# Kernel tuning notes

Measured on AMD Instinct MI355X. Metric: run time of the kernel, lower is better.

## Reference

```python
import jax, jax.numpy as jnp
import numpy as np

EPS_LN = 1e-12
EPS_BN = 1e-5


def layernorm(x, w, b):
    u = jnp.mean(x, axis=-1, keepdims=True)
    s = jnp.mean((x - u) ** 2, axis=-1, keepdims=True)
    return w * ((x - u) / jnp.sqrt(s + EPS_LN)) + b


def reps_block(x, ln1_w, ln1_b, lin_w, lin_b, ln2_w, ln2_b):
    # GRAPHLayerNorm -> (dropout, identity in eval) -> Linear -> ReLU -> GRAPHLayerNorm
    h = layernorm(x, ln1_w, ln1_b)
    h = jax.nn.relu(jnp.einsum('bnd,od->bno', h, lin_w) + lin_b)
    return layernorm(h, ln2_w, ln2_b)


def attend(x):
    # full dense self-attention: softmax(x x^T) x ; dropout is identity in eval
    scores = jnp.einsum('bnd,bmd->bnm', x, x)  # [B,4096,4096]
    attn = jax.nn.softmax(scores, axis=-1)
    return jnp.einsum('bnm,bmd->bnd', attn, x)


def setup_inputs() -> dict:
    key = jax.random.key(0)
    ks = jax.random.split(key, 8)
    B, C, H, W = 4, 512, 64, 64
    D = 512
    inp = {
        'T1': jax.random.normal(ks[0], (B, C, H, W), jnp.float32),
        'T2': jax.random.normal(ks[1], (B, C, H, W), jnp.float32),
        'w_conv3': jax.random.normal(ks[2], (1024, 1024, 3, 3), jnp.float32) * 0.01,
        'w_conv1': jax.random.normal(ks[3], (512, 1024, 1, 1), jnp.float32) * 0.03,
        'bn_gamma': jnp.ones((512,), jnp.float32),
        'bn_beta': jnp.zeros((512,), jnp.float32),
        'bn_mean': jnp.zeros((512,), jnp.float32),
        'bn_var': jnp.ones((512,), jnp.float32),
        'ln1_w': jnp.ones((D,), jnp.float32),
        'ln1_b': jnp.zeros((D,), jnp.float32),
        'lin_w': jax.random.normal(ks[4], (D, D), jnp.float32) * 0.04,
        'lin_b': jnp.zeros((D,), jnp.float32),
        'ln2_w': jnp.ones((D,), jnp.float32),
        'ln2_b': jnp.zeros((D,), jnp.float32),
    }
    return inp


def reference(T1, T2, w_conv3, w_conv1, bn_gamma, bn_beta, bn_mean, bn_var,
              ln1_w, ln1_b, lin_w, lin_b, ln2_w, ln2_b):
    B = T1.shape[0]
    X = jnp.concatenate((T1, T2), axis=1)  # [B,1024,64,64]
    dn = ('NCHW', 'OIHW', 'NCHW')
    X = jax.lax.conv_general_dilated(X, w_conv3, (1, 1), ((1, 1), (1, 1)), dimension_numbers=dn)
    X = jax.lax.conv_general_dilated(X, w_conv1, (1, 1), ((0, 0), (0, 0)), dimension_numbers=dn)  # [B,512,64,64]
    # BatchNorm (eval, running stats) + ReLU
    inv = (bn_gamma / jnp.sqrt(bn_var + EPS_BN))[None, :, None, None]
    X = jax.nn.relu(X * inv + (bn_beta - bn_mean * bn_gamma / jnp.sqrt(bn_var + EPS_BN))[None, :, None, None])
    x = X.transpose(0, 2, 3, 1).reshape(B, 4096, 512)
    # block 1
    rel = attend(x)
    rel = reps_block(x + rel, ln1_w, ln1_b, lin_w, lin_b, ln2_w, ln2_b)
    # block 2 (original code reuses self.reps_graph, i.e. SAME params)
    rel1 = attend(rel)
    rel1 = reps_block(rel + rel1, ln1_w, ln1_b, lin_w, lin_b, ln2_w, ln2_b)
    return rel1.reshape(B, 64, 64, 512).transpose(0, 3, 1, 2)  # [B,512,64,64]
```

## Files before the change

kernel.cpp:

```cpp
#include <hip/hip_runtime.h>
#include <stdint.h>

typedef float f32x4 __attribute__((ext_vector_type(4)));
typedef __bf16 bf16x8 __attribute__((ext_vector_type(8)));
typedef unsigned short u16;
typedef unsigned short u16x8 __attribute__((ext_vector_type(8)));

__device__ __forceinline__ float bf2f(u16 u){ unsigned int i = ((unsigned int)u)<<16; float f; __builtin_memcpy(&f,&i,4); return f; }
__device__ __forceinline__ u16 f2bf(float f){ unsigned int i; __builtin_memcpy(&i,&f,4); i += 0x7FFFu + ((i>>16)&1u); return (u16)(i>>16); }
__device__ __forceinline__ u16 f2h(float f){ _Float16 h = (_Float16)f; u16 b; __builtin_memcpy(&b,&h,2); return b; }
__device__ __forceinline__ float h2f(u16 b){ _Float16 h; __builtin_memcpy(&h,&b,2); return (float)h; }

__device__ __forceinline__ void gld16(const void* g, void* l){
  __builtin_amdgcn_global_load_lds(
      (const __attribute__((address_space(1))) void*)(uintptr_t)g,
      (__attribute__((address_space(3))) void*)(unsigned int)(uintptr_t)l, 16, 0, 0);
}

__global__ __launch_bounds__(256) void border_zero(u16* __restrict__ Xpad){
  const int n = blockIdx.y, p = blockIdx.x;
  int y, x;
  if (p < 66)        { y = 0;        x = p; }
  else if (p < 132)  { y = 65;       x = p - 66; }
  else if (p < 196)  { y = p - 131;  x = 0; }
  else               { y = p - 195;  x = 65; }
  ushort4 z = {0,0,0,0};
  *(ushort4*)(Xpad + (((long)n*66 + y)*66 + x)*1024 + threadIdx.x*4) = z;
}

__global__ __launch_bounds__(256) void pad_interior(const float* __restrict__ T1,
                                                    const float* __restrict__ T2,
                                                    u16* __restrict__ Xpad){
  const int n = blockIdx.z, ct = blockIdx.y, pt = blockIdx.x;
  const int t = threadIdx.x;
  const int c0 = ct*64, p0 = pt*64;
  const float* src = (c0 < 512) ? (T1 + ((long)n*512 + c0)*4096)
                                : (T2 + ((long)n*512 + (c0-512))*4096);
  __shared__ u16 lds[64][66];
  #pragma unroll
  for (int i=0;i<4;i++){
    int c = i*16 + (t>>4);
    int ch = t&15;
    float4 v = *(const float4*)(src + (long)c*4096 + p0 + ch*4);
    int p = ch*4;
    lds[p+0][c] = f2bf(v.x); lds[p+1][c] = f2bf(v.y);
    lds[p+2][c] = f2bf(v.z); lds[p+3][c] = f2bf(v.w);
  }
  __syncthreads();
  #pragma unroll
  for (int i=0;i<8;i++){
    int p = i*8 + (t>>5);
    int c2 = t&31;
    int pix = p0 + p; int yy = (pix>>6)+1, xx = (pix&63)+1;
    ushort2 val; val.x = lds[p][2*c2]; val.y = lds[p][2*c2+1];
    *(ushort2*)(Xpad + (((long)n*66 + yy)*66 + xx)*1024 + c0 + 2*c2) = val;
  }
}

__global__ __launch_bounds__(256) void prep_w3(const float* __restrict__ w3, u16* __restrict__ wk3t){
  const int o = blockIdx.x; const int t = threadIdx.x;
  __shared__ u16 lds[9216];
  const float* src = w3 + (long)o*9216;
  #pragma unroll
  for (int i=0;i<9;i++){
    int j = i*256 + t;
    float4 v = *(const float4*)(src + j*4);
    lds[j*4+0]=f2bf(v.x); lds[j*4+1]=f2bf(v.y); lds[j*4+2]=f2bf(v.z); lds[j*4+3]=f2bf(v.w);
  }
  __syncthreads();
  u16* dst = wk3t + (long)o*9216;
  #pragma unroll
  for (int i=0;i<36;i++){
    int j = i*256 + t; int tp = j>>10, ci = j&1023;
    dst[j] = lds[ci*9+tp];
  }
}

__global__ void prep_small(const float* __restrict__ w1, const float* __restrict__ bg,
                           const float* __restrict__ bb, const float* __restrict__ bm,
                           const float* __restrict__ bv, const float* __restrict__ linw,
                           u16* __restrict__ w1t, u16* __restrict__ lint,
                           float* __restrict__ bias1){
  const int b = blockIdx.x, t = threadIdx.x;
  if (b < 2048){
    long i = (long)b*256 + t;
    int o = (int)(i>>10);
    float inv = bg[o] / sqrtf(bv[o] + 1e-5f);
    w1t[i] = f2bf(w1[i]*inv);
  } else if (b < 3072){
    long i = (long)(b-2048)*256 + t;
    lint[i] = f2bf(linw[i]);
  } else {
    int o = (b-3072)*256 + t;
    float inv = bg[o]/sqrtf(bv[o]+1e-5f);
    bias1[o] = bb[o] - bm[o]*inv;
  }
}

__global__ __launch_bounds__(256) void row_norm(const u16* __restrict__ x, float* __restrict__ nrm){
  const int row = blockIdx.x*4 + (threadIdx.x>>6);
  const int lane = threadIdx.x & 63;
  u16x8 q = *(const u16x8*)(x + (long)row*512 + lane*8);
  float s = 0.f;
  #pragma unroll
  for (int j=0;j<8;j++){ float f = bf2f(q[j]); s += f*f; }
  #pragma unroll
  for (int off=32; off; off>>=1) s += __shfl_xor(s, off);
  if (lane==0) nrm[row] = s;
}

__global__ __launch_bounds__(256) void transpose_bf(const u16* __restrict__ src, u16* __restrict__ dst,
                                                    int R, int C, long sStr, long dStr){
  const int z = blockIdx.z;
  src += (long)z*sStr; dst += (long)z*dStr;
  const int r0 = blockIdx.x*64, c0 = blockIdx.y*64;
  const int t = threadIdx.x;
  __shared__ u16 lds[64][66];
  #pragma unroll
  for (int i=0;i<4;i++){
    int r = i*16 + (t>>4), ch = t&15;
    ushort4 v = *(const ushort4*)(src + (long)(r0+r)*C + c0 + ch*4);
    lds[r][ch*4+0]=v.x; lds[r][ch*4+1]=v.y; lds[r][ch*4+2]=v.z; lds[r][ch*4+3]=v.w;
  }
  __syncthreads();
  #pragma unroll
  for (int i=0;i<4;i++){
    int c = i*16 + (t>>4), ch = t&15;
    ushort4 v;
    v.x = lds[ch*4+0][c]; v.y = lds[ch*4+1][c]; v.z = lds[ch*4+2][c]; v.w = lds[ch*4+3][c];
    *(ushort4*)(dst + (long)(c0+c)*R + r0 + ch*4) = v;
  }
}

__global__ __launch_bounds__(256) void transpose_bf_f32(const u16* __restrict__ src, float* __restrict__ dst){
  const int z = blockIdx.z;
  src += (long)z*4096*512; dst += (long)z*512*4096;
  const int r0 = blockIdx.x*64, c0 = blockIdx.y*64;
  const int t = threadIdx.x;
  __shared__ u16 lds[64][66];
  #pragma unroll
  for (int i=0;i<4;i++){
    int r = i*16 + (t>>4), ch = t&15;
    ushort4 v = *(const ushort4*)(src + (long)(r0+r)*512 + c0 + ch*4);
    lds[r][ch*4+0]=v.x; lds[r][ch*4+1]=v.y; lds[r][ch*4+2]=v.z; lds[r][ch*4+3]=v.w;
  }
  __syncthreads();
  #pragma unroll
  for (int i=0;i<4;i++){
    int c = i*16 + (t>>4), ch = t&15;
    float4 v;
    v.x = bf2f(lds[ch*4+0][c]); v.y = bf2f(lds[ch*4+1][c]);
    v.z = bf2f(lds[ch*4+2][c]); v.w = bf2f(lds[ch*4+3][c]);
    *(float4*)(dst + (long)(c0+c)*4096 + r0 + ch*4) = v;
  }
}

template<int EPI, int CONV>
__global__ __launch_bounds__(512, 2) void gemm256(
    const u16* __restrict__ Ain, const u16* __restrict__ Btin, void* __restrict__ Cv,
    int K, int lda, int ldb, int ldc, const float* __restrict__ srowIn,
    u16* __restrict__ C0, u16* __restrict__ C1, u16* __restrict__ C2, u16* __restrict__ C3)
{
  extern __shared__ u16 sm[];
  const int t = threadIdx.x;
  const int lane = t & 63;
  const int wid = t >> 6;
  const int wr = wid >> 2, wc = wid & 3;

  long m0, n0;
  int byv = 0, bxv = 0;
  const u16* A; const u16* Bt; const float* srow; u16* Cz;
  if (EPI == 3){
    const int orig = blockIdx.x;
    const int swz = (orig & 7) * 68 + (orig >> 3);
    const int z = swz / 136;
    int p = swz % 136;
    int by = 0;
    while (p >= 16 - by){ p -= 16 - by; by++; }
    const int bx = by + p;
    byv = by; bxv = bx;
    m0 = (long)by * 256; n0 = (long)bx * 256;
    A = Ain + (long)z*4096*lda;
    Bt = A;
    srow = srowIn + (long)z*4096;
    Cz = (z==0)?C0:(z==1)?C1:(z==2)?C2:C3;
  } else {
    const int orig = blockIdx.y * gridDim.x + blockIdx.x;
    const int cpx = (gridDim.x * gridDim.y) >> 3;
    const int swz = (orig & 7) * cpx + (orig >> 3);
    const int bx = swz % gridDim.x;
    const int by = swz / gridDim.x;
    m0 = (long)by * 256; n0 = (long)bx * 256;
    A = Ain; Bt = Btin; srow = srowIn; Cz = (u16*)Cv;
  }

  const int row0 = t >> 2;
  const int cs0  = (t & 3) ^ ((row0 >> 1) & 3);

  const u16 *aB0, *aB1;
  if (CONV) {
    long m_ = m0 + row0;
    long pb0 = ((long)((int)(m_>>12)*66 + (int)((m_>>6)&63)))*66 + (int)(m_&63);
    m_ = m0 + row0 + 128;
    long pb1 = ((long)((int)(m_>>12)*66 + (int)((m_>>6)&63)))*66 + (int)(m_&63);
    aB0 = A + pb0*1024 + cs0*8;
    aB1 = A + pb1*1024 + cs0*8;
  } else {
    aB0 = A + (m0 + row0)*(long)lda + cs0*8;
    aB1 = A + (m0 + row0 + 128)*(long)lda + cs0*8;
  }
  const u16* bB0 = Bt + (n0 + row0)*(long)ldb + cs0*8;
  const u16* bB1 = Bt + (n0 + row0 + 128)*(long)ldb + cs0*8;

  auto issueA = [&](int sub, long aoff){
    u16* d = sm + sub*8192 + t*8;
    gld16(aB0 + aoff, d);
    gld16(aB1 + aoff, d + 4096);
  };
  auto issueB = [&](int sub, long boff){
    u16* d = sm + 32768 + sub*8192 + t*8;
    gld16(bB0 + boff, d);
    gld16(bB1 + boff, d + 4096);
  };
  auto conv_aoff = [&](int tile)->long {
    int kb = tile << 6;
    int tap = kb >> 10;
    int cb  = kb & 1023;
    int ky = (tap >= 6) ? 2 : (tap >= 3 ? 1 : 0);
    int kx = tap - ky*3;
    return (long)(ky*66 + kx)*1024 + cb;
  };

  const int frow = lane & 15;
  const int elemoff = (((lane>>4) ^ ((frow>>1)&3)) << 3);
  const int rAoff = (wr*128 + frow)*32 + elemoff;
  const int rBoff = (wc*64  + frow)*32 + elemoff;

  f32x4 acc[8][4] = {};

  {
    long a0 = CONV ? conv_aoff(0) : 0L;
    issueA(0, a0);
    issueB(0, 0);
    issueA(1, a0 + 32);
    issueB(1, 32);
  }

  const int NT = K >> 6;
  for (int tile = 0; tile < NT; ++tile) {
    const int b = tile & 1;
    const int nb2 = b ^ 1;
    const bool lastT = (tile == NT-1);
    long aoffN = 0, boffN = 0;
    if (!lastT) {
      aoffN = CONV ? conv_aoff(tile+1) : (long)(tile+1)*64;
      boffN = (long)(tile+1)*64;
    }

    asm volatile("s_waitcnt vmcnt(4)" ::: "memory");
    __builtin_amdgcn_s_barrier();
    __builtin_amdgcn_sched_barrier(0);

    {
      const u16* pA = sm + (b*2+0)*8192 + rAoff;
      const u16* pB = sm + 32768 + (b*2+0)*8192 + rBoff;
      bf16x8 bf[4];
      #pragma unroll
      for (int i=0;i<4;i++) bf[i] = *(const bf16x8*)(pB + i*512);
      {
        bf16x8 a[4];
        #pragma unroll
        for (int i=0;i<4;i++) a[i] = *(const bf16x8*)(pA + i*512);
        if (!lastT) issueA(nb2*2+0, aoffN);
        __builtin_amdgcn_s_setprio(1);
        #pragma unroll
        for (int mi=0;mi<4;mi++)
          #pragma unroll
          for (int ni=0;ni<4;ni++)
            acc[mi][ni] = __builtin_amdgcn_mfma_f32_16x16x32_bf16(a[mi], bf[ni], acc[mi][ni],0,0,0);
        __builtin_amdgcn_s_setprio(0);
      }
      {
        bf16x8 a[4];
        #pragma unroll
        for (int i=0;i<4;i++) a[i] = *(const bf16x8*)(pA + (4+i)*512);
        if (!lastT) issueB(nb2*2+0, boffN);
        __builtin_amdgcn_s_setprio(1);
        #pragma unroll
        for (int mi=0;mi<4;mi++)
          #pragma unroll
          for (int ni=0;ni<4;ni++)
            acc[4+mi][ni] = __builtin_amdgcn_mfma_f32_16x16x32_bf16(a[mi], bf[ni], acc[4+mi][ni],0,0,0);
        __builtin_amdgcn_s_setprio(0);
      }
    }

    if (lastT) asm volatile("s_waitcnt vmcnt(0)" ::: "memory");
    else       asm volatile("s_waitcnt vmcnt(4)" ::: "memory");
    __builtin_amdgcn_s_barrier();
    __builtin_amdgcn_sched_barrier(0);

    {
      const u16* pA = sm + (b*2+1)*8192 + rAoff;
      const u16* pB = sm + 32768 + (b*2+1)*8192 + rBoff;
      bf16x8 bf[4];
      #pragma unroll
      for (int i=0;i<4;i++) bf[i] = *(const bf16x8*)(pB + i*512);
      {
        bf16x8 a[4];
        #pragma unroll
        for (int i=0;i<4;i++) a[i] = *(const bf16x8*)(pA + i*512);
        if (!lastT) issueA(nb2*2+1, aoffN + 32);
        __builtin_amdgcn_s_setprio(1);
        #pragma unroll
        for (int mi=0;mi<4;mi++)
          #pragma unroll
          for (int ni=0;ni<4;ni++)
            acc[mi][ni] = __builtin_amdgcn_mfma_f32_16x16x32_bf16(a[mi], bf[ni], acc[mi][ni],0,0,0);
        __builtin_amdgcn_s_setprio(0);
      }
      {
        bf16x8 a[4];
        #pragma unroll
        for (int i=0;i<4;i++) a[i] = *(const bf16x8*)(pA + (4+i)*512);
        if (!lastT) issueB(nb2*2+1, boffN + 32);
        __builtin_amdgcn_s_setprio(1);
        #pragma unroll
        for (int mi=0;mi<4;mi++)
          #pragma unroll
          for (int ni=0;ni<4;ni++)
            acc[4+mi][ni] = __builtin_amdgcn_mfma_f32_16x16x32_bf16(a[mi], bf[ni], acc[4+mi][ni],0,0,0);
        __builtin_amdgcn_s_setprio(0);
      }
    }
  }

  const int crow0 = wr*128 + ((lane>>4)<<2);
  const int ccol0 = wc*64 + frow;

  #pragma unroll
  for (int mi=0;mi<8;mi++){
    #pragma unroll
    for (int ni=0;ni<4;ni++){
      long col = n0 + ccol0 + ni*16;
      #pragma unroll
      for (int r=0;r<4;r++){
        long row = m0 + crow0 + mi*16 + r;
        float v = acc[mi][ni][r];
        if (EPI==3) Cz[row*(long)ldc + col] = f2h(v - srow[row]);
        else        Cz[row*(long)ldc + col] = f2bf(v);
      }
    }
  }

  if (EPI == 3 && bxv != byv){
    __syncthreads();
    u16* lt = sm;
    float sc[4];
    #pragma unroll
    for (int ni=0;ni<4;ni++) sc[ni] = srow[n0 + ccol0 + ni*16];
    #pragma unroll
    for (int mi=0;mi<8;mi++){
      const int g = (crow0 + mi*16) >> 2;
      #pragma unroll
      for (int ni=0;ni<4;ni++){
        const int col_l = ccol0 + ni*16;
        ushort4 pk;
        #pragma unroll
        for (int r=0;r<4;r++) pk[r] = f2h(acc[mi][ni][r] - sc[ni]);
        *(ushort4*)(lt + col_l*256 + ((g ^ (col_l & 63))<<2)) = pk;
      }
    }
    __syncthreads();
    const int half = lane >> 5, l32 = lane & 31;
    #pragma unroll
    for (int ps=0; ps<16; ps++){
      const int R = ps*16 + wid*2 + half;
      const int u0 = ((l32<<1)    ) ^ (R & 63);
      const int u1 = ((l32<<1) | 1) ^ (R & 63);
      ushort4 a = *(const ushort4*)(lt + R*256 + (u0<<2));
      ushort4 b = *(const ushort4*)(lt + R*256 + (u1<<2));
      u16* dst = Cz + (n0 + R)*(long)ldc + m0 + (l32<<3);
      *(ushort4*)dst = a;
      *(ushort4*)(dst+4) = b;
    }
  }
}

template<int EPI>
__global__ __launch_bounds__(256, 2) void gemm128_deep(
    const u16* __restrict__ A, const u16* __restrict__ Bt, u16* __restrict__ C,
    const float* __restrict__ bias, int K, int lda, int ldb, int ldc)
{
  extern __shared__ u16 pm[];
  const int L = blockIdx.x;
  const int xcd = L & 7;
  const int q = L >> 3;
  const int by = (q >> 2) + xcd*16;
  const int bx = q & 3;
  const long m0 = (long)by * 128, n0 = (long)bx * 128;

  const int t = threadIdx.x;
  const int lane = t & 63;
  const int w = t >> 6;
  const int wr = w >> 1, wc = w & 1;

  const int row0 = t >> 2;
  const int cs0  = (t & 3) ^ ((row0 >> 1) & 3);

  const u16* aB0 = A + (m0 + row0)*(long)lda + cs0*8;
  const u16* aB1 = aB0 + 64*(long)lda;
  const u16* bB0 = Bt + (n0 + row0)*(long)ldb + cs0*8;
  const u16* bB1 = bB0 + 64*(long)ldb;

  auto issueA = [&](int sub, long off){
    u16* d = pm + sub*4096 + t*8;
    gld16(aB0 + off, d);
    gld16(aB1 + off, d + 2048);
  };
  auto issueB = [&](int sub, long off){
    u16* d = pm + 16384 + sub*4096 + t*8;
    gld16(bB0 + off, d);
    gld16(bB1 + off, d + 2048);
  };

  const int frow = lane & 15;
  const int elemoff = (((lane>>4) ^ ((frow>>1)&3)) << 3);
  const int rAoff = (wr*64 + frow)*32 + elemoff;
  const int rBoff = (wc*64 + frow)*32 + elemoff;

  f32x4 acc[4][4] = {};

  issueA(0, 0);  issueB(0, 0);
  issueA(1, 32); issueB(1, 32);

  const int NT = K >> 6;
  for (int tl = 0; tl < NT; ++tl) {
    const int b = tl & 1;
    const int nb2 = b ^ 1;
    const bool lastT = (tl == NT-1);
    const long offN = (long)(tl+1)*64;

    asm volatile("s_waitcnt vmcnt(4)" ::: "memory");
    __builtin_amdgcn_s_barrier();
    __builtin_amdgcn_sched_barrier(0);

    {
      const u16* pA = pm + (b*2+0)*4096 + rAoff;
      const u16* pB = pm + 16384 + (b*2+0)*4096 + rBoff;
      bf16x8 bf[4];
      #pragma unroll
      for (int i=0;i<4;i++) bf[i] = *(const bf16x8*)(pB + i*512);
      {
        bf16x8 a[2];
        #pragma unroll
        for (int i=0;i<2;i++) a[i] = *(const bf16x8*)(pA + i*512);
        if (!lastT) issueA(nb2*2+0, offN);
        __builtin_amdgcn_s_setprio(1);
        #pragma unroll
        for (int mi=0;mi<2;mi++)
          #pragma unroll
          for (int ni=0;ni<4;ni++)
            acc[mi][ni] = __builtin_amdgcn_mfma_f32_16x16x32_bf16(a[mi], bf[ni], acc[mi][ni],0,0,0);
        __builtin_amdgcn_s_setprio(0);
      }
      {
        bf16x8 a[2];
        #pragma unroll
        for (int i=0;i<2;i++) a[i] = *(const bf16x8*)(pA + (2+i)*512);
        if (!lastT) issueB(nb2*2+0, offN);
        __builtin_amdgcn_s_setprio(1);
        #pragma unroll
        for (int mi=0;mi<2;mi++)
          #pragma unroll
          for (int ni=0;ni<4;ni++)
            acc[2+mi][ni] = __builtin_amdgcn_mfma_f32_16x16x32_bf16(a[mi], bf[ni], acc[2+mi][ni],0,0,0);
        __builtin_amdgcn_s_setprio(0);
      }
    }

    if (lastT) asm volatile("s_waitcnt vmcnt(0)" ::: "memory");
    else       asm volatile("s_waitcnt vmcnt(4)" ::: "memory");
    __builtin_amdgcn_s_barrier();
    __builtin_amdgcn_sched_barrier(0);

    {
      const u16* pA = pm + (b*2+1)*4096 + rAoff;
      const u16* pB = pm + 16384 + (b*2+1)*4096 + rBoff;
      bf16x8 bf[4];
      #pragma unroll
      for (int i=0;i<4;i++) bf[i] = *(const bf16x8*)(pB + i*512);
      {
        bf16x8 a[2];
        #pragma unroll
        for (int i=0;i<2;i++) a[i] = *(const bf16x8*)(pA + i*512);
        if (!lastT) issueA(nb2*2+1, offN + 32);
        __builtin_amdgcn_s_setprio(1);
        #pragma unroll
        for (int mi=0;mi<2;mi++)
          #pragma unroll
          for (int ni=0;ni<4;ni++)
            acc[mi][ni] = __builtin_amdgcn_mfma_f32_16x16x32_bf16(a[mi], bf[ni], acc[mi][ni],0,0,0);
        __builtin_amdgcn_s_setprio(0);
      }
      {
        bf16x8 a[2];
        #pragma unroll
        for (int i=0;i<2;i++) a[i] = *(const bf16x8*)(pA + (2+i)*512);
        if (!lastT) issueB(nb2*2+1, offN + 32);
        __builtin_amdgcn_s_setprio(1);
        #pragma unroll
        for (int mi=0;mi<2;mi++)
          #pragma unroll
          for (int ni=0;ni<4;ni++)
            acc[2+mi][ni] = __builtin_amdgcn_mfma_f32_16x16x32_bf16(a[mi], bf[ni], acc[2+mi][ni],0,0,0);
        __builtin_amdgcn_s_setprio(0);
      }
    }
  }

  const int crow0 = wr*64 + ((lane>>4)<<2);
  const int ccol0 = wc*64 + frow;
  #pragma unroll
  for (int mi=0;mi<4;mi++){
    #pragma unroll
    for (int ni=0;ni<4;ni++){
      long col = n0 + ccol0 + ni*16;
      float bv = (EPI==1) ? bias[col] : 0.0f;
      #pragma unroll
      for (int r=0;r<4;r++){
        long row = m0 + crow0 + mi*16 + r;
        float v = acc[mi][ni][r];
        if (EPI==1){ v += bv; v = v > 0.0f ? v : 0.0f; }
        C[row*(long)ldc + col] = f2bf(v);
      }
    }
  }
}

__global__ __launch_bounds__(256, 2) void pv5(
    const u16* __restrict__ P0, const u16* __restrict__ P1,
    const u16* __restrict__ P2, const u16* __restrict__ P3,
    const u16* __restrict__ xT, u16* __restrict__ attb)
{
  extern __shared__ u16 pm[];
  const int L = blockIdx.x;
  const int xcd = L & 7;
  const int z = xcd >> 1;
  const int q = L >> 3;
  const int by = ((q >> 2) << 1) + (xcd & 1);
  const int bx = q & 3;
  const long ZS = 4096L*512;
  const u16* A  = (z==0)?P0:(z==1)?P1:(z==2)?P2:P3;
  const u16* Bt = xT   + (long)z*ZS;
  u16*       C  = attb + (long)z*ZS;
  const long m0 = (long)by * 128, n0 = (long)bx * 128;

  const int t = threadIdx.x;
  const int lane = t & 63;
  const int w = t >> 6;
  const int wr = w >> 1, wc = w & 1;

  const int row0 = t >> 2;
  const int cs0  = (t & 3) ^ ((row0 >> 1) & 3);

  const u16* aB0 = A + (m0 + row0)*4096L + cs0*8;
  const u16* aB1 = aB0 + 64*4096L;
  const u16* bB0 = Bt + (n0 + row0)*4096L + cs0*8;
  const u16* bB1 = bB0 + 64*4096L;

  auto issueA = [&](int sub, long off){
    u16* d = pm + sub*4096 + t*8;
    gld16(aB0 + off, d);
    gld16(aB1 + off, d + 2048);
  };
  auto issueB = [&](int sub, long off){
    u16* d = pm + 16384 + sub*4096 + t*8;
    gld16(bB0 + off, d);
    gld16(bB1 + off, d + 2048);
  };

  const int frow = lane & 15;
  const int elemoff = (((lane>>4) ^ ((frow>>1)&3)) << 3);
  const int rAoff = (wr*64 + frow)*32 + elemoff;
  const int rBoff = (wc*64 + frow)*32 + elemoff;

  f32x4 acc[4][4] = {};

  issueA(0, 0);  issueB(0, 0);
  issueA(1, 32); issueB(1, 32);

  const int NT = 64;
  for (int tl = 0; tl < NT; ++tl) {
    const int b = tl & 1;
    const int nb2 = b ^ 1;
    const bool lastT = (tl == NT-1);
    const long offN = (long)(tl+1)*64;

    asm volatile("s_waitcnt vmcnt(4)" ::: "memory");
    __builtin_amdgcn_s_barrier();
    __builtin_amdgcn_sched_barrier(0);

    {
      const u16* pA = pm + (b*2+0)*4096 + rAoff;
      const u16* pB = pm + 16384 + (b*2+0)*4096 + rBoff;
      bf16x8 bf[4];
      #pragma unroll
      for (int i=0;i<4;i++) bf[i] = *(const bf16x8*)(pB + i*512);
      {
        bf16x8 a[2];
        #pragma unroll
        for (int i=0;i<2;i++) a[i] = *(const bf16x8*)(pA + i*512);
        if (!lastT) issueA(nb2*2+0, offN);
        __builtin_amdgcn_s_setprio(1);
        #pragma unroll
        for (int mi=0;mi<2;mi++)
          #pragma unroll
          for (int ni=0;ni<4;ni++)
            acc[mi][ni] = __builtin_amdgcn_mfma_f32_16x16x32_bf16(a[mi], bf[ni], acc[mi][ni],0,0,0);
        __builtin_amdgcn_s_setprio(0);
      }
      {
        bf16x8 a[2];
        #pragma unroll
        for (int i=0;i<2;i++) a[i] = *(const bf16x8*)(pA + (2+i)*512);
        if (!lastT) issueB(nb2*2+0, offN);
        __builtin_amdgcn_s_setprio(1);
        #pragma unroll
        for (int mi=0;mi<2;mi++)
          #pragma unroll
          for (int ni=0;ni<4;ni++)
            acc[2+mi][ni] = __builtin_amdgcn_mfma_f32_16x16x32_bf16(a[mi], bf[ni], acc[2+mi][ni],0,0,0);
        __builtin_amdgcn_s_setprio(0);
      }
    }

    if (lastT) asm volatile("s_waitcnt vmcnt(0)" ::: "memory");
    else       asm volatile("s_waitcnt vmcnt(4)" ::: "memory");
    __builtin_amdgcn_s_barrier();
    __builtin_amdgcn_sched_barrier(0);

    {
      const u16* pA = pm + (b*2+1)*4096 + rAoff;
      const u16* pB = pm + 16384 + (b*2+1)*4096 + rBoff;
      bf16x8 bf[4];
      #pragma unroll
      for (int i=0;i<4;i++) bf[i] = *(const bf16x8*)(pB + i*512);
      {
        bf16x8 a[2];
        #pragma unroll
        for (int i=0;i<2;i++) a[i] = *(const bf16x8*)(pA + i*512);
        if (!lastT) issueA(nb2*2+1, offN + 32);
        __builtin_amdgcn_s_setprio(1);
        #pragma unroll
        for (int mi=0;mi<2;mi++)
          #pragma unroll
          for (int ni=0;ni<4;ni++)
            acc[mi][ni] = __builtin_amdgcn_mfma_f32_16x16x32_bf16(a[mi], bf[ni], acc[mi][ni],0,0,0);
        __builtin_amdgcn_s_setprio(0);
      }
      {
        bf16x8 a[2];
        #pragma unroll
        for (int i=0;i<2;i++) a[i] = *(const bf16x8*)(pA + (2+i)*512);
        if (!lastT) issueB(nb2*2+1, offN + 32);
        __builtin_amdgcn_s_setprio(1);
        #pragma unroll
        for (int mi=0;mi<2;mi++)
          #pragma unroll
          for (int ni=0;ni<4;ni++)
            acc[2+mi][ni] = __builtin_amdgcn_mfma_f32_16x16x32_bf16(a[mi], bf[ni], acc[2+mi][ni],0,0,0);
        __builtin_amdgcn_s_setprio(0);
      }
    }
  }

  const int crow0 = wr*64 + ((lane>>4)<<2);
  const int ccol0 = wc*64 + frow;
  #pragma unroll
  for (int mi=0;mi<4;mi++){
    #pragma unroll
    for (int ni=0;ni<4;ni++){
      long col = n0 + ccol0 + ni*16;
      #pragma unroll
      for (int r=0;r<4;r++){
        long row = m0 + crow0 + mi*16 + r;
        C[row*512 + col] = f2bf(acc[mi][ni][r]);
      }
    }
  }
}

__global__ __launch_bounds__(256) void softmax_batched(
    u16* __restrict__ S0, u16* __restrict__ S1,
    u16* __restrict__ S2, u16* __restrict__ S3)
{
  const int z = blockIdx.x >> 12;
  const long row = blockIdx.x & 4095;
  u16* buf = (z==0)?S0:(z==1)?S1:(z==2)?S2:S3;
  u16* src = buf + row*4096;
  const int t = threadIdx.x, lane = t&63, w = t>>6;
  float v[16];
  #pragma unroll
  for (int i=0;i<2;i++){
    u16x8 q = *(const u16x8*)(src + t*16 + i*8);
    #pragma unroll
    for (int j=0;j<8;j++) v[i*8+j] = h2f(q[j]);
  }
  float mx = v[0];
  #pragma unroll
  for (int i=1;i<16;i++) mx = fmaxf(mx, v[i]);
  #pragma unroll
  for (int off=32; off; off>>=1) mx = fmaxf(mx, __shfl_xor(mx, off));
  __shared__ float red[4];
  if (lane==0) red[w] = mx;
  __syncthreads();
  mx = fmaxf(fmaxf(red[0],red[1]), fmaxf(red[2],red[3]));
  float sum = 0.0f;
  #pragma unroll
  for (int i=0;i<16;i++){ v[i] = __expf(v[i]-mx); sum += v[i]; }
  #pragma unroll
  for (int off=32; off; off>>=1) sum += __shfl_xor(sum, off);
  __shared__ float red2[4];
  if (lane==0) red2[w] = sum;
  __syncthreads();
  sum = red2[0]+red2[1]+red2[2]+red2[3];
  const float inv = 1.0f/sum;
  #pragma unroll
  for (int i=0;i<2;i++){
    u16x8 o;
    #pragma unroll
    for (int j=0;j<8;j++) o[j] = f2bf(v[i*8+j]*inv);
    *(u16x8*)(src + t*16 + i*8) = o;
  }
}

template<int ADD>
__global__ __launch_bounds__(256) void ln_row(
    const u16* __restrict__ X, const u16* __restrict__ Y,
    const float* __restrict__ w, const float* __restrict__ b,
    u16* __restrict__ outB)
{
  const long row = blockIdx.x;
  const int t = threadIdx.x, lane = t&63, wv = t>>6;
  ushort2 xv = *(const ushort2*)(X + row*512 + t*2);
  float v0 = bf2f(xv.x), v1 = bf2f(xv.y);
  if (ADD){
    ushort2 yv = *(const ushort2*)(Y + row*512 + t*2);
    v0 += bf2f(yv.x); v1 += bf2f(yv.y);
  }
  float s = v0+v1, q = v0*v0 + v1*v1;
  #pragma unroll
  for (int off=32; off; off>>=1){ s += __shfl_xor(s,off); q += __shfl_xor(q,off); }
  __shared__ float red[8];
  if (lane==0){ red[wv]=s; red[4+wv]=q; }
  __syncthreads();
  s = red[0]+red[1]+red[2]+red[3];
  q = red[4]+red[5]+red[6]+red[7];
  const float u = s*(1.0f/512.0f);
  const float var = q*(1.0f/512.0f) - u*u;
  const float inv = rsqrtf(var + 1e-12f);
  const int c = t*2;
  float o0 = (v0-u)*inv*w[c]   + b[c];
  float o1 = (v1-u)*inv*w[c+1] + b[c+1];
  ushort2 ov; ov.x=f2bf(o0); ov.y=f2bf(o1);
  *(ushort2*)(outB + row*512 + c) = ov;
}

extern "C" void kernel_launch(void* const* d_in, const int* in_sizes, int n_in,
                              void* d_out, int out_size, void* d_ws, size_t ws_size,
                              hipStream_t stream) {
  const float* T1   = (const float*)d_in[0];
  const float* T2   = (const float*)d_in[1];
  const float* w3   = (const float*)d_in[2];
  const float* w1   = (const float*)d_in[3];
  const float* bg   = (const float*)d_in[4];
  const float* bb   = (const float*)d_in[5];
  const float* bm   = (const float*)d_in[6];
  const float* bv   = (const float*)d_in[7];
  const float* ln1w = (const float*)d_in[8];
  const float* ln1b = (const float*)d_in[9];
  const float* linw = (const float*)d_in[10];
  const float* linb = (const float*)d_in[11];
  const float* ln2w = (const float*)d_in[12];
  const float* ln2b = (const float*)d_in[13];

  hipFuncSetAttribute(reinterpret_cast<const void*>(gemm256<0,1>),
                      hipFuncAttributeMaxDynamicSharedMemorySize, 131072);
  hipFuncSetAttribute(reinterpret_cast<const void*>(gemm256<3,0>),
                      hipFuncAttributeMaxDynamicSharedMemorySize, 131072);
  hipFuncSetAttribute(reinterpret_cast<const void*>(pv5),
                      hipFuncAttributeMaxDynamicSharedMemorySize, 65536);
  hipFuncSetAttribute(reinterpret_cast<const void*>(gemm128_deep<0>),
                      hipFuncAttributeMaxDynamicSharedMemorySize, 65536);
  hipFuncSetAttribute(reinterpret_cast<const void*>(gemm128_deep<1>),
                      hipFuncAttributeMaxDynamicSharedMemorySize, 65536);

  char* ws = (char*)d_ws;
  size_t off = 0;
  auto alloc = [&](size_t bytes)->char* {
    char* p = ws + off;
    off += (bytes + 255) & ~(size_t)255;
    return p;
  };
  const size_t XPAD_B = 4L*66*66*1024*2;
  u16*   Xpad  = (u16*)  alloc(XPAD_B);
  u16*   wk3t  = (u16*)  alloc(1024L*9216*2);
  u16*   w1t   = (u16*)  alloc(512L*1024*2);
  u16*   lint  = (u16*)  alloc(512L*512*2);
  float* bias1 = (float*)alloc(512*4);
  float* nrm   = (float*)alloc(16384L*4);
  u16*   Y1    = (u16*)  alloc(16384L*1024*2);
  u16*   x0    = (u16*)  alloc(16384L*512*2);
  u16*   xT    = (u16*)  alloc(4L*512*4096*2);
  u16*   Sreg  = (u16*)  alloc(2L*4096*4096*2);
  u16*   attb  = (u16*)  alloc(16384L*512*2);
  u16*   h     = (u16*)  alloc(16384L*512*2);
  u16*   g     = (u16*)  alloc(16384L*512*2);
  u16*   rel1  = (u16*)  alloc(16384L*512*2);
  u16*   S0    = Y1;
  u16*   S1    = Sreg;
  u16*   S2    = Sreg + 4096L*4096;
  u16*   S3    = Xpad;
  if (off > ws_size) return;

  const long ZS = 4096L*512;

  border_zero<<<dim3(260,4), 256, 0, stream>>>(Xpad);
  pad_interior<<<dim3(64,16,4), 256, 0, stream>>>(T1, T2, Xpad);
  prep_w3<<<1024, 256, 0, stream>>>(w3, wk3t);
  prep_small<<<3074, 256, 0, stream>>>(w1, bg, bb, bm, bv, linw, w1t, lint, bias1);

  gemm256<0,1><<<dim3(4,64), 512, 131072, stream>>>(Xpad, wk3t, (void*)Y1, 9216, 0, 9216, 1024,
                                                    nullptr, nullptr, nullptr, nullptr, nullptr);
  gemm128_deep<1><<<512, 256, 65536, stream>>>(Y1, w1t, x0, bias1, 1024, 1024, 1024, 512);

  auto attend = [&](const u16* xin){
    transpose_bf<<<dim3(64,8,4), 256, 0, stream>>>(xin, xT, 4096, 512, ZS, ZS);
    row_norm<<<4096, 256, 0, stream>>>(xin, nrm);
    gemm256<3,0><<<dim3(544), 512, 131072, stream>>>(xin, xin, nullptr, 512, 512, 512, 4096,
                                                     nrm, S0, S1, S2, S3);
    softmax_batched<<<16384, 256, 0, stream>>>(S0, S1, S2, S3);
    pv5<<<512, 256, 65536, stream>>>(S0, S1, S2, S3, xT, attb);
  };

  attend(x0);
  ln_row<1><<<16384, 256, 0, stream>>>(x0, attb, ln1w, ln1b, h);
  gemm128_deep<1><<<512, 256, 65536, stream>>>(h, lint, g, linb, 512, 512, 512, 512);
  ln_row<0><<<16384, 256, 0, stream>>>(g, nullptr, ln2w, ln2b, rel1);

  attend(rel1);
  ln_row<1><<<16384, 256, 0, stream>>>(rel1, attb, ln1w, ln1b, h);
  gemm128_deep<1><<<512, 256, 65536, stream>>>(h, lint, g, linb, 512, 512, 512, 512);
  ln_row<0><<<16384, 256, 0, stream>>>(g, nullptr, ln2w, ln2b, x0);

  transpose_bf_f32<<<dim3(64,8,4), 256, 0, stream>>>(x0, (float*)d_out);
}
```

Baseline: 794.9 us.

## Replace 256-tile symmetric score GEMM with 128-tile kernel mapped per XCD

```diff
diff --git a/kernel.cpp b/kernel.cpp
--- a/kernel.cpp
+++ b/kernel.cpp
@@ -158,8 +158,7 @@
 template<int EPI, int CONV>
 __global__ __launch_bounds__(512, 2) void gemm256(
     const u16* __restrict__ Ain, const u16* __restrict__ Btin, void* __restrict__ Cv,
-    int K, int lda, int ldb, int ldc, const float* __restrict__ srowIn,
-    u16* __restrict__ C0, u16* __restrict__ C1, u16* __restrict__ C2, u16* __restrict__ C3)
+    int K, int lda, int ldb, int ldc)
 {
   extern __shared__ u16 sm[];
   const int t = threadIdx.x;
@@ -167,32 +166,13 @@
   const int wid = t >> 6;
   const int wr = wid >> 2, wc = wid & 3;
 
-  long m0, n0;
-  int byv = 0, bxv = 0;
-  const u16* A; const u16* Bt; const float* srow; u16* Cz;
-  if (EPI == 3){
-    const int orig = blockIdx.x;
-    const int swz = (orig & 7) * 68 + (orig >> 3);
-    const int z = swz / 136;
-    int p = swz % 136;
-    int by = 0;
-    while (p >= 16 - by){ p -= 16 - by; by++; }
-    const int bx = by + p;
-    byv = by; bxv = bx;
-    m0 = (long)by * 256; n0 = (long)bx * 256;
-    A = Ain + (long)z*4096*lda;
-    Bt = A;
-    srow = srowIn + (long)z*4096;
-    Cz = (z==0)?C0:(z==1)?C1:(z==2)?C2:C3;
-  } else {
-    const int orig = blockIdx.y * gridDim.x + blockIdx.x;
-    const int cpx = (gridDim.x * gridDim.y) >> 3;
-    const int swz = (orig & 7) * cpx + (orig >> 3);
-    const int bx = swz % gridDim.x;
-    const int by = swz / gridDim.x;
-    m0 = (long)by * 256; n0 = (long)bx * 256;
-    A = Ain; Bt = Btin; srow = srowIn; Cz = (u16*)Cv;
-  }
+  const int orig = blockIdx.y * gridDim.x + blockIdx.x;
+  const int cpx = (gridDim.x * gridDim.y) >> 3;
+  const int swz = (orig & 7) * cpx + (orig >> 3);
+  const int bx = swz % gridDim.x;
+  const int by = swz / gridDim.x;
+  const long m0 = (long)by * 256, n0 = (long)bx * 256;
+  const u16* A = Ain; const u16* Bt = Btin; u16* Cz = (u16*)Cv;
 
   const int row0 = t >> 2;
   const int cs0  = (t & 3) ^ ((row0 >> 1) & 3);
@@ -337,7 +317,6 @@
 
   const int crow0 = wr*128 + ((lane>>4)<<2);
   const int ccol0 = wc*64 + frow;
-
   #pragma unroll
   for (int mi=0;mi<8;mi++){
     #pragma unroll
@@ -346,21 +325,174 @@
       #pragma unroll
       for (int r=0;r<4;r++){
         long row = m0 + crow0 + mi*16 + r;
-        float v = acc[mi][ni][r];
-        if (EPI==3) Cz[row*(long)ldc + col] = f2h(v - srow[row]);
-        else        Cz[row*(long)ldc + col] = f2bf(v);
-      }
-    }
-  }
-
-  if (EPI == 3 && bxv != byv){
+        Cz[row*(long)ldc + col] = f2bf(acc[mi][ni][r]);
+      }
+    }
+  }
+}
+
+__global__ __launch_bounds__(256, 2) void s_gemm128(
+    const u16* __restrict__ xin, const float* __restrict__ srowIn,
+    u16* __restrict__ C0, u16* __restrict__ C1, u16* __restrict__ C2, u16* __restrict__ C3)
+{
+  extern __shared__ u16 pm[];
+  const int L = blockIdx.x;
+  const int xcd = L & 7;
+  const int z = xcd >> 1;
+  const int tid = (xcd & 1)*264 + (L >> 3);
+  int p = tid, by = 0;
+  while (p >= 32 - by){ p -= 32 - by; by++; }
+  const int bx = by + p;
+  const long m0 = (long)by * 128, n0 = (long)bx * 128;
+
+  const u16* A = xin + (long)z*4096*512;
+  const float* srow = srowIn + (long)z*4096;
+  u16* Cz = (z==0)?C0:(z==1)?C1:(z==2)?C2:C3;
+  const int ldc = 4096;
+
+  const int t = threadIdx.x;
+  const int lane = t & 63;
+  const int w = t >> 6;
+  const int wr = w >> 1, wc = w & 1;
+
+  const int row0 = t >> 2;
+  const int cs0  = (t & 3) ^ ((row0 >> 1) & 3);
+
+  const u16* aB0 = A + (m0 + row0)*512L + cs0*8;
+  const u16* aB1 = aB0 + 64*512L;
+  const u16* bB0 = A + (n0 + row0)*512L + cs0*8;
+  const u16* bB1 = bB0 + 64*512L;
+
+  auto issueA = [&](int sub, long off){
+    u16* d = pm + sub*4096 + t*8;
+    gld16(aB0 + off, d);
+    gld16(aB1 + off, d + 2048);
+  };
+  auto issueB = [&](int sub, long off){
+    u16* d = pm + 16384 + sub*4096 + t*8;
+    gld16(bB0 + off, d);
+    gld16(bB1 + off, d + 2048);
+  };
+
+  const int frow = lane & 15;
+  const int elemoff = (((lane>>4) ^ ((frow>>1)&3)) << 3);
+  const int rAoff = (wr*64 + frow)*32 + elemoff;
+  const int rBoff = (wc*64 + frow)*32 + elemoff;
+
+  f32x4 acc[4][4] = {};
+
+  issueA(0, 0);  issueB(0, 0);
+  issueA(1, 32); issueB(1, 32);
+
+  const int NT = 8;
+  for (int tl = 0; tl < NT; ++tl) {
+    const int b = tl & 1;
+    const int nb2 = b ^ 1;
+    const bool lastT = (tl == NT-1);
+    const long offN = (long)(tl+1)*64;
+
+    asm volatile("s_waitcnt vmcnt(4)" ::: "memory");
+    __builtin_amdgcn_s_barrier();
+    __builtin_amdgcn_sched_barrier(0);
+
+    {
+      const u16* pA = pm + (b*2+0)*4096 + rAoff;
+      const u16* pB = pm + 16384 + (b*2+0)*4096 + rBoff;
+      bf16x8 bf[4];
+      #pragma unroll
+      for (int i=0;i<4;i++) bf[i] = *(const bf16x8*)(pB + i*512);
+      {
+        bf16x8 a[2];
+        #pragma unroll
+        for (int i=0;i<2;i++) a[i] = *(const bf16x8*)(pA + i*512);
+        if (!lastT) issueA(nb2*2+0, offN);
+        __builtin_amdgcn_s_setprio(1);
+        #pragma unroll
+        for (int mi=0;mi<2;mi++)
+          #pragma unroll
+          for (int ni=0;ni<4;ni++)
+            acc[mi][ni] = __builtin_amdgcn_mfma_f32_16x16x32_bf16(a[mi], bf[ni], acc[mi][ni],0,0,0);
+        __builtin_amdgcn_s_setprio(0);
+      }
+      {
+        bf16x8 a[2];
+        #pragma unroll
+        for (int i=0;i<2;i++) a[i] = *(const bf16x8*)(pA + (2+i)*512);
+        if (!lastT) issueB(nb2*2+0, offN);
+        __builtin_amdgcn_s_setprio(1);
+        #pragma unroll
+        for (int mi=0;mi<2;mi++)
+          #pragma unroll
+          for (int ni=0;ni<4;ni++)
+            acc[2+mi][ni] = __builtin_amdgcn_mfma_f32_16x16x32_bf16(a[mi], bf[ni], acc[2+mi][ni],0,0,0);
+        __builtin_amdgcn_s_setprio(0);
+      }
+    }
+
+    if (lastT) asm volatile("s_waitcnt vmcnt(0)" ::: "memory");
+    else       asm volatile("s_waitcnt vmcnt(4)" ::: "memory");
+    __builtin_amdgcn_s_barrier();
+    __builtin_amdgcn_sched_barrier(0);
+
+    {
+      const u16* pA = pm + (b*2+1)*4096 + rAoff;
+      const u16* pB = pm + 16384 + (b*2+1)*4096 + rBoff;
+      bf16x8 bf[4];
+      #pragma unroll
+      for (int i=0;i<4;i++) bf[i] = *(const bf16x8*)(pB + i*512);
+      {
+        bf16x8 a[2];
+        #pragma unroll
+        for (int i=0;i<2;i++) a[i] = *(const bf16x8*)(pA + i*512);
+        if (!lastT) issueA(nb2*2+1, offN + 32);
+        __builtin_amdgcn_s_setprio(1);
+        #pragma unroll
+        for (int mi=0;mi<2;mi++)
+          #pragma unroll
+          for (int ni=0;ni<4;ni++)
+            acc[mi][ni] = __builtin_amdgcn_mfma_f32_16x16x32_bf16(a[mi], bf[ni], acc[mi][ni],0,0,0);
+        __builtin_amdgcn_s_setprio(0);
+      }
+      {
+        bf16x8 a[2];
+        #pragma unroll
+        for (int i=0;i<2;i++) a[i] = *(const bf16x8*)(pA + (2+i)*512);
+        if (!lastT) issueB(nb2*2+1, offN + 32);
+        __builtin_amdgcn_s_setprio(1);
+        #pragma unroll
+        for (int mi=0;mi<2;mi++)
+          #pragma unroll
+          for (int ni=0;ni<4;ni++)
+            acc[2+mi][ni] = __builtin_amdgcn_mfma_f32_16x16x32_bf16(a[mi], bf[ni], acc[2+mi][ni],0,0,0);
+        __builtin_amdgcn_s_setprio(0);
+      }
+    }
+  }
+
+  const int crow0 = wr*64 + ((lane>>4)<<2);
+  const int ccol0 = wc*64 + frow;
+
+  #pragma unroll
+  for (int mi=0;mi<4;mi++){
+    #pragma unroll
+    for (int r=0;r<4;r++){
+      long row = m0 + crow0 + mi*16 + r;
+      float sr = srow[row];
+      u16* cb = Cz + row*(long)ldc + n0 + ccol0;
+      #pragma unroll
+      for (int ni=0;ni<4;ni++)
+        cb[ni*16] = f2h(acc[mi][ni][r] - sr);
+    }
+  }
+
+  if (bx != by){
     __syncthreads();
-    u16* lt = sm;
+    u16* lt = pm;
     float sc[4];
     #pragma unroll
     for (int ni=0;ni<4;ni++) sc[ni] = srow[n0 + ccol0 + ni*16];
     #pragma unroll
-    for (int mi=0;mi<8;mi++){
+    for (int mi=0;mi<4;mi++){
       const int g = (crow0 + mi*16) >> 2;
       #pragma unroll
       for (int ni=0;ni<4;ni++){
@@ -368,21 +500,17 @@
         ushort4 pk;
         #pragma unroll
         for (int r=0;r<4;r++) pk[r] = f2h(acc[mi][ni][r] - sc[ni]);
-        *(ushort4*)(lt + col_l*256 + ((g ^ (col_l & 63))<<2)) = pk;
+        *(ushort4*)(lt + col_l*128 + ((g ^ (col_l & 31))<<2)) = pk;
       }
     }
     __syncthreads();
     const int half = lane >> 5, l32 = lane & 31;
     #pragma unroll
     for (int ps=0; ps<16; ps++){
-      const int R = ps*16 + wid*2 + half;
-      const int u0 = ((l32<<1)    ) ^ (R & 63);
-      const int u1 = ((l32<<1) | 1) ^ (R & 63);
-      ushort4 a = *(const ushort4*)(lt + R*256 + (u0<<2));
-      ushort4 b = *(const ushort4*)(lt + R*256 + (u1<<2));
-      u16* dst = Cz + (n0 + R)*(long)ldc + m0 + (l32<<3);
-      *(ushort4*)dst = a;
-      *(ushort4*)(dst+4) = b;
+      const int R = ps*8 + w*2 + half;
+      const int u = l32 ^ (R & 31);
+      ushort4 a = *(const ushort4*)(lt + R*128 + (u<<2));
+      *(ushort4*)(Cz + (n0 + R)*(long)ldc + m0 + (l32<<2)) = a;
     }
   }
 }
@@ -787,8 +915,8 @@
 
   hipFuncSetAttribute(reinterpret_cast<const void*>(gemm256<0,1>),
                       hipFuncAttributeMaxDynamicSharedMemorySize, 131072);
-  hipFuncSetAttribute(reinterpret_cast<const void*>(gemm256<3,0>),
-                      hipFuncAttributeMaxDynamicSharedMemorySize, 131072);
+  hipFuncSetAttribute(reinterpret_cast<const void*>(s_gemm128),
+                      hipFuncAttributeMaxDynamicSharedMemorySize, 65536);
   hipFuncSetAttribute(reinterpret_cast<const void*>(pv5),
                       hipFuncAttributeMaxDynamicSharedMemorySize, 65536);
   hipFuncSetAttribute(reinterpret_cast<const void*>(gemm128_deep<0>),
@@ -831,15 +959,13 @@
   prep_w3<<<1024, 256, 0, stream>>>(w3, wk3t);
   prep_small<<<3074, 256, 0, stream>>>(w1, bg, bb, bm, bv, linw, w1t, lint, bias1);
 
-  gemm256<0,1><<<dim3(4,64), 512, 131072, stream>>>(Xpad, wk3t, (void*)Y1, 9216, 0, 9216, 1024,
-                                                    nullptr, nullptr, nullptr, nullptr, nullptr);
+  gemm256<0,1><<<dim3(4,64), 512, 131072, stream>>>(Xpad, wk3t, (void*)Y1, 9216, 0, 9216, 1024);
   gemm128_deep<1><<<512, 256, 65536, stream>>>(Y1, w1t, x0, bias1, 1024, 1024, 1024, 512);
 
   auto attend = [&](const u16* xin){
     transpose_bf<<<dim3(64,8,4), 256, 0, stream>>>(xin, xT, 4096, 512, ZS, ZS);
     row_norm<<<4096, 256, 0, stream>>>(xin, nrm);
-    gemm256<3,0><<<dim3(544), 512, 131072, stream>>>(xin, xin, nullptr, 512, 512, 512, 4096,
-                                                     nrm, S0, S1, S2, S3);
+    s_gemm128<<<2112, 256, 65536, stream>>>(xin, nrm, S0, S1, S2, S3);
     softmax_batched<<<16384, 256, 0, stream>>>(S0, S1, S2, S3);
     pv5<<<512, 256, 65536, stream>>>(S0, S1, S2, S3, xT, attb);
   };
```

New measurement: 784.6 us (median of 2 runs). About the same (-1.3%).
